# Kernel optimization log

Measured on AMD Instinct MI355X. Metric: run time of the kernel, lower is better.

The kernel has to match this reference:

```python
import jax, jax.numpy as jnp
import numpy as np

NL, H, PD, NH, NB = 4, 256, 64, 4, 65
B, L, AA = 2, 384, 48
DH = H // NH
MAX_REL = 32


def _ln(x, g, b):
    m = x.mean(-1, keepdims=True)
    v = ((x - m) ** 2).mean(-1, keepdims=True)
    return (x - m) * jax.lax.rsqrt(v + 1e-5) * g + b


def setup_inputs() -> dict:
    key = jax.random.key(0)
    ks = iter(jax.random.split(key, 64))
    w = lambda *s: jax.random.normal(next(ks), s, jnp.float32) * 0.02
    return dict(
        x=jax.random.normal(next(ks), (B, L, AA), jnp.float32),
        rp_w=w(AA, H), rp_b=jnp.zeros((H,), jnp.float32),
        pos_embed=w(L, H),
        pii_w=w(H, PD), pii_b=jnp.zeros((PD,), jnp.float32),
        pij_w=w(H, PD), pij_b=jnp.zeros((PD,), jnp.float32),
        rel_emb=w(2 * MAX_REL + 2, PD),
        ln_seq_g=jnp.ones((NL, H), jnp.float32), ln_seq_b=jnp.zeros((NL, H), jnp.float32),
        ln_pair_g=jnp.ones((NL, PD), jnp.float32), ln_pair_b=jnp.zeros((NL, PD), jnp.float32),
        pb_w=w(NL, PD, NH),
        in_w=w(NL, H, 3 * H), in_b=jnp.zeros((NL, 3 * H), jnp.float32),
        out_w=w(NL, H, H), out_b=jnp.zeros((NL, H), jnp.float32),
        ff_ln_g=jnp.ones((NL, H), jnp.float32), ff_ln_b=jnp.zeros((NL, H), jnp.float32),
        ff_w1=w(NL, H, 4 * H), ff_b1=jnp.zeros((NL, 4 * H), jnp.float32),
        ff_w2=w(NL, 4 * H, H), ff_b2=jnp.zeros((NL, H), jnp.float32),
        pu_ln_g=jnp.ones((NL, PD), jnp.float32), pu_ln_b=jnp.zeros((NL, PD), jnp.float32),
        pu_w1=w(NL, PD, PD), pu_b1=jnp.zeros((NL, PD), jnp.float32),
        pu_w2=w(NL, PD, PD), pu_b2=jnp.zeros((NL, PD), jnp.float32),
        outer_w=w(NL, 2 * H, PD), outer_b=jnp.zeros((NL, PD), jnp.float32),
        dh_ln_g=jnp.ones((PD,), jnp.float32), dh_ln_b=jnp.zeros((PD,), jnp.float32),
        dh_w1=w(PD, PD), dh_b1=jnp.zeros((PD,), jnp.float32),
        dh_w2=w(PD, NB), dh_b2=jnp.zeros((NB,), jnp.float32),
    )


def reference(x, rp_w, rp_b, pos_embed, pii_w, pii_b, pij_w, pij_b, rel_emb,
              ln_seq_g, ln_seq_b, ln_pair_g, ln_pair_b, pb_w, in_w, in_b,
              out_w, out_b, ff_ln_g, ff_ln_b, ff_w1, ff_b1, ff_w2, ff_b2,
              pu_ln_g, pu_ln_b, pu_w1, pu_b1, pu_w2, pu_b2, outer_w, outer_b,
              dh_ln_g, dh_ln_b, dh_w1, dh_b1, dh_w2, dh_b2):
    Bx, Lx, _ = x.shape
    gelu = lambda t: jax.nn.gelu(t, approximate=False)  # torch nn.GELU default (erf)
    h = x @ rp_w + rp_b + pos_embed[:Lx][None]
    # pair init: outer sum of two linear projections + clipped rel-pos embedding
    pair = (h @ pii_w + pii_b)[:, :, None, :] + (h @ pij_w + pij_b)[:, None, :, :]
    idx = jnp.arange(Lx)
    rel = jnp.clip(idx[None, :] - idx[:, None], -MAX_REL, MAX_REL) + MAX_REL  # (L,L)
    pair = pair + rel_emb[rel][None]
    for i in range(NL):
        seq_n = _ln(h, ln_seq_g[i], ln_seq_b[i])
        bias = _ln(pair, ln_pair_g[i], ln_pair_b[i]) @ pb_w[i]  # (B,L,L,NH)
        mask = bias.mean(axis=(0, 3))  # torch: permute->reshape(B*NH,L,L)->mean(0)
        qkv = seq_n @ in_w[i] + in_b[i]
        q, k, v = jnp.split(qkv, 3, axis=-1)
        q = q.reshape(Bx, Lx, NH, DH)
        k = k.reshape(Bx, Lx, NH, DH)
        v = v.reshape(Bx, Lx, NH, DH)
        scores = jnp.einsum('blhd,bmhd->bhlm', q, k) / float(np.sqrt(DH)) + mask
        attn = jax.nn.softmax(scores, axis=-1)
        o = jnp.einsum('bhlm,bmhd->blhd', attn, v).reshape(Bx, Lx, H)
        h = h + o @ out_w[i] + out_b[i]
        h = h + gelu(_ln(h, ff_ln_g[i], ff_ln_b[i]) @ ff_w1[i] + ff_b1[i]) @ ff_w2[i] + ff_b2[i]
        # outer_proj(cat([h_i, h_j])) == h@W[:H] outer-summed with h@W[H:]
        oi = h @ outer_w[i][:H]
        oj = h @ outer_w[i][H:]
        outer = oi[:, :, None, :] + oj[:, None, :, :] + outer_b[i]  # (B,L,L,PD)
        pair = pair + gelu(_ln(outer, pu_ln_g[i], pu_ln_b[i]) @ pu_w1[i] + pu_b1[i]) @ pu_w2[i] + pu_b2[i]
    logits = gelu(_ln(pair, dh_ln_g, dh_ln_b) @ dh_w1 + dh_b1) @ dh_w2 + dh_b2
    return (logits + jnp.swapaxes(logits, 1, 2)) / 2.0
```

## Files before the change

### kernel.cpp

```cpp
#include <hip/hip_runtime.h>
#include <math.h>

#define LSEQ 384
#define HD 256
#define PDIM 64
#define NHEAD 4
#define NBINS 65
#define BATCH 2
#define NTT (LSEQ / 16)
#define NTRI (NTT * (NTT + 1) / 2)

typedef __attribute__((ext_vector_type(8))) short bf16x8;
typedef __attribute__((ext_vector_type(16))) float f32x16;
#define MFMA32(a, b, c) __builtin_amdgcn_mfma_f32_32x32x16_bf16(a, b, c, 0, 0, 0)

template<int CTRL, int RMASK>
__device__ __forceinline__ float dpp_sum_step(float v) {
    int x = __builtin_amdgcn_update_dpp(0, __float_as_int(v), CTRL, RMASK, 0xf, true);
    return v + __int_as_float(x);
}
template<int CTRL, int RMASK>
__device__ __forceinline__ float dpp_max_step(float v) {
    int x = __builtin_amdgcn_update_dpp(__float_as_int(v), __float_as_int(v), CTRL, RMASK, 0xf, false);
    return fmaxf(v, __int_as_float(x));
// ... 42 lines not shown
    int t = threadIdx.x;
    if (t < 48) xs[t] = x[row * 48 + t];
    __syncthreads();
    float acc = rp_b[t] + pos[l * HD + t];
#pragma unroll 8
    for (int a = 0; a < 48; ++a) acc += xs[a] * rp_w[a * HD + t];
    h[row * HD + t] = acc;
}

__global__ void k_proj2(const float* __restrict__ h, const float* __restrict__ wA,
                        const float* __restrict__ wB, const float* __restrict__ bA,
                        const float* __restrict__ bB, int center,
                        float* __restrict__ pA, float* __restrict__ pB) {
    __shared__ float hs[HD];
    int row = blockIdx.x;
    int t = threadIdx.x;
    hs[t] = h[row * HD + t];
    hs[t + 128] = h[row * HD + t + 128];
    __syncthreads();
    int col = t & 63;
    const float* w = (t < 64) ? wA : wB;
    const float* bias = (t < 64) ? bA : bB;
    float acc = bias ? bias[col] : 0.0f;
#pragma unroll 8
    for (int a = 0; a < HD; ++a) acc += hs[a] * w[a * PDIM + col];
    if (center) {
        float mean = wsum(acc) * (1.0f / PDIM);
        acc -= mean;
    }
    float* p = (t < 64) ? pA : pB;
    p[row * PDIM + col] = acc;
}

__global__ void k_pair_init(const float* __restrict__ pi, const float* __restrict__ pj,
                            const float* __restrict__ rel_emb, float* __restrict__ pair) {
    __shared__ float pis[PDIM];
    int row = blockIdx.x;
    int b = row / LSEQ, i = row % LSEQ;
    int t = threadIdx.x;
    if (t < PDIM) pis[t] = pi[row * PDIM + t];
    __syncthreads();
    const float* pjb = pj + (size_t)b * LSEQ * PDIM;
    float* pr = pair + (size_t)row * LSEQ * PDIM;
    for (int n = t; n < LSEQ * PDIM; n += 256) {
        int j = n >> 6, d = n & 63;
        int r = j - i; r = r < -32 ? -32 : (r > 32 ? 32 : r); r += 32;
        pr[n] = pis[d] + pjb[j * PDIM + d] + rel_emb[r * PDIM + d];
    }
}

__global__ void k_prep(const float* __restrict__ pu_ln_g, const float* __restrict__ pu_ln_b,
                       const float* __restrict__ pu_w1, const float* __restrict__ pu_b1,
                       const float* __restrict__ pu_w2,
                       const float* __restrict__ dh_ln_g, const float* __restrict__ dh_ln_b,
                       const float* __restrict__ dh_w1, const float* __restrict__ dh_b1,
                       const float* __restrict__ dh_w2,
                       unsigned short* __restrict__ w1hT, unsigned short* __restrict__ w1lT,
                       unsigned short* __restrict__ w2hT, unsigned short* __restrict__ w2lT,
                       float* __restrict__ b1p, float* __restrict__ w2c) {
    int i = blockIdx.x;
    int c = threadIdx.x;
    const float *g, *bb, *w1, *b1, *w2;
    int w2s;
    if (i < 4) { g = pu_ln_g + i * 64; bb = pu_ln_b + i * 64; w1 = pu_w1 + i * 4096;
                 b1 = pu_b1 + i * 64; w2 = pu_w2 + i * 4096; w2s = 64; }
    else       { g = dh_ln_g; bb = dh_ln_b; w1 = dh_w1; b1 = dh_b1; w2 = dh_w2; w2s = 65; }
    float accb = b1[c];
    for (int k = 0; k < 64; ++k) {
        float wv = w1[k * 64 + c];
        accb += bb[k] * wv;
        unsigned short h, l;
        split_bf(g[k] * wv, h, l);
        w1hT[i * 4096 + c * 64 + k] = h;
        w1lT[i * 4096 + c * 64 + k] = l;
        split_bf(w2[k * w2s + c], h, l);
        w2hT[i * 4096 + c * 64 + k] = h;
        w2lT[i * 4096 + c * 64 + k] = l;
    }
    b1p[i * 64 + c] = accb;
    if (i == 4) w2c[c] = dh_w2[c * 65 + 64];
}

__global__ void k_maskprep(const float* __restrict__ g, const float* __restrict__ bb,
                           const float* __restrict__ pbw, float* __restrict__ gp,
                           float* __restrict__ cb) {
    int li = blockIdx.x + 1;
    int c = threadIdx.x;
    const float* pw = pbw + li * PDIM * NHEAD;
    float pbs = pw[c * 4] + pw[c * 4 + 1] + pw[c * 4 + 2] + pw[c * 4 + 3];
    gp[blockIdx.x * 64 + c] = g[li * 64 + c] * pbs;
    float s = wsum(bb[li * 64 + c] * pbs);
    if (c == 0) cb[blockIdx.x] = s;
}

__global__ void k_split_T(const float* __restrict__ src, unsigned short* __restrict__ dh,
                          unsigned short* __restrict__ dl, int K, int N,
                          int tiles_k, int tiles_n, size_t sstride, size_t dstride) {
    __shared__ float lds[64][65];
    int bid = blockIdx.x;
    int tpl = tiles_k * tiles_n;
    int layer = bid / tpl;
    int rest = bid % tpl;
    int kt = rest / tiles_n, nt = rest % tiles_n;
    const float* s = src + layer * sstride;
    int t = threadIdx.x, c = t & 63, r0 = t >> 6;
    for (int r = r0; r < 64; r += 4)
        lds[r][c] = s[(size_t)(kt * 64 + r) * N + nt * 64 + c];
    __syncthreads();
    unsigned short* oh = dh + layer * dstride;
    unsigned short* ol = dl + layer * dstride;
    for (int r = r0; r < 64; r += 4) {
        float v = lds[c][r];
        unsigned short h, l;
        split_bf(v, h, l);
        size_t o = (size_t)(nt * 64 + r) * K + kt * 64 + c;
        oh[o] = h;
        ol[o] = l;
    }
}

template<bool GELU>
__global__ void __launch_bounds__(256) k_gemm(
    const float* __restrict__ X, const unsigned short* __restrict__ wTh,
    const unsigned short* __restrict__ wTl, const float* __restrict__ bias,
    const float* __restrict__ R, float* __restrict__ OUT, int K, int N) {
// ... 6 lines not shown
    const unsigned short* bh = wTh + (size_t)(nt * 32 + pl) * K + 8 * hq;
    const unsigned short* bl = wTl + (size_t)(nt * 32 + pl) * K + 8 * hq;
    int n = nt * 32 + pl;
    float bv = bias[n];
    f32x16 acc;
#pragma unroll
    for (int r = 0; r < 16; ++r) {
        int mr = mt * 32 + (r & 3) + 8 * (r >> 2) + 4 * hq;
        acc[r] = bv + (R ? R[(size_t)mr * N + n] : 0.0f);
    }
#pragma unroll 4
    for (int s = 0; s < K; s += 16) {
        bf16x8 ah, al;
#pragma unroll
        for (int j = 0; j < 8; ++j) {
            unsigned short h, l;
            split_bf(xr[s + j], h, l);
            ah[j] = (short)h; al[j] = (short)l;
        }
        bf16x8 bhv = *(const bf16x8*)(bh + s);
        bf16x8 blv = *(const bf16x8*)(bl + s);
        acc = MFMA32(ah, bhv, acc);
        acc = MFMA32(al, bhv, acc);
        acc = MFMA32(ah, blv, acc);
    }
#pragma unroll
    for (int r = 0; r < 16; ++r) {
        int mr = mt * 32 + (r & 3) + 8 * (r >> 2) + 4 * hq;
        float v = acc[r];
        OUT[(size_t)mr * N + n] = GELU ? gelu_erf(v) : v;
    }
}

__global__ void k_mask(const float* __restrict__ pair, const float* __restrict__ g,
                       const float* __restrict__ bb, const float* __restrict__ pbw,
                       float* __restrict__ mask) {
    int wid = (blockIdx.x * 4 + (threadIdx.x >> 6)) * 2;
    int lane = threadIdx.x & 63;
    int l = wid / LSEQ, m0 = wid % LSEQ;
    float gd = g[lane], bd = bb[lane];
    float pbs = pbw[lane * 4] + pbw[lane * 4 + 1] + pbw[lane * 4 + 2] + pbw[lane * 4 + 3];
    float v[4];
#pragma unroll
    for (int s = 0; s < 4; ++s) {
        int b = s >> 1, m = m0 + (s & 1);
        v[s] = pair[(((size_t)(b * LSEQ + l)) * LSEQ + m) * PDIM + lane];
    }
    float mean[4], d[4], var[4], dot[4];
#pragma unroll
    for (int s = 0; s < 4; ++s) mean[s] = wsum(v[s]) * (1.0f / PDIM);
#pragma unroll
    for (int s = 0; s < 4; ++s) d[s] = v[s] - mean[s];
#pragma unroll
    for (int s = 0; s < 4; ++s) var[s] = wsum(d[s] * d[s]) * (1.0f / PDIM);
#pragma unroll
    for (int s = 0; s < 4; ++s) {
        float ln = d[s] * rsqrtf(var[s] + 1e-5f) * gd + bd;
        dot[s] = wsum(ln * pbs);
    }
    if (lane == 0) {
        mask[l * LSEQ + m0]     = (dot[0] + dot[2]) * (1.0f / (BATCH * NHEAD));
        mask[l * LSEQ + m0 + 1] = (dot[1] + dot[3]) * (1.0f / (BATCH * NHEAD));
    }
}

__global__ void k_ln_seq(const float* __restrict__ h, const float* __restrict__ g,
                         const float* __restrict__ b, float* __restrict__ out) {
    __shared__ float red[8];
    int row = blockIdx.x;
    int t = threadIdx.x;
    int w = t >> 6, lane = t & 63;
    float v = h[row * HD + t];
    float s = wsum(v);
    if (lane == 0) red[w] = s;
    __syncthreads();
    float mean = (red[0] + red[1] + red[2] + red[3]) * (1.0f / HD);
    float d = v - mean;
    float q = wsum(d * d);
    if (lane == 0) red[4 + w] = q;
    __syncthreads();
    float var = (red[4] + red[5] + red[6] + red[7]) * (1.0f / HD);
    out[row * HD + t] = d * rsqrtf(var + 1e-5f) * g[t] + b[t];
}

__global__ void k_attn(const float* __restrict__ qkv, const float* __restrict__ mask,
                       float* __restrict__ o) {
    __shared__ __align__(16) float qs[64];
    __shared__ float sc[LSEQ];
    __shared__ float red[8];
    __shared__ float op[4][64];
    int bid = blockIdx.x;
    int l = bid % LSEQ;
    int nh = (bid / LSEQ) & 3;
    int b = bid / (LSEQ * NHEAD);
    int t = threadIdx.x;
    int w = t >> 6, lane = t & 63;
    const float* qbase = qkv + ((size_t)(b * LSEQ + l)) * 768 + nh * 64;
    if (t < 64) qs[t] = qbase[t];
// ... 18 lines not shown
            lmax = fmaxf(lmax, s);
        } else myv[it] = -1e30f;
    }
    float wm = wmax(lmax);
    if (lane == 0) red[w] = wm;
    __syncthreads();
    float gmax = fmaxf(fmaxf(red[0], red[1]), fmaxf(red[2], red[3]));
    float lsum = 0.0f;
#pragma unroll
    for (int it = 0; it < 2; ++it) {
        int m = t + it * 256;
        if (m < LSEQ) {
            float e = expf(myv[it] - gmax);
            sc[m] = e;
            lsum += e;
        }
    }
    float ws = wsum(lsum);
    if (lane == 0) red[4 + w] = ws;
    __syncthreads();
    float inv = 1.0f / (red[4] + red[5] + red[6] + red[7]);
    int d = t & 63, gq = t >> 6;
    float part = 0.0f;
    for (int m = gq * 96; m < (gq + 1) * 96; ++m)
        part += sc[m] * qkv[((size_t)(b * LSEQ + m)) * 768 + 512 + nh * 64 + d];
    op[gq][d] = part;
    __syncthreads();
    if (t < 64) {
        float ov = (op[0][t] + op[1][t] + op[2][t] + op[3][t]) * inv;
        o[((size_t)(b * LSEQ + l)) * HD + nh * 64 + t] = ov;
    }
}

__global__ void __launch_bounds__(256) k_pair_upd(
    const float* __restrict__ ojc,
    const float* __restrict__ oic,
    const unsigned short* __restrict__ w1hT, const unsigned short* __restrict__ w1lT,
    const float* __restrict__ b1p,
    const unsigned short* __restrict__ w2hT, const unsigned short* __restrict__ w2lT,
    const float* __restrict__ b2, float* __restrict__ pair,
    const float* __restrict__ gpb, const float* __restrict__ cbv,
    float* __restrict__ mask_out) {
    __shared__ float pt[128][65];
    __shared__ float gpl[64];
    int blk = blockIdx.x;
    int row = blk / 3, seg = blk % 3;
    int b = row / LSEQ;
    int t = threadIdx.x;
    int wave = t >> 6, lane = t & 63;
    int pl = lane & 31, hq = lane >> 5;
    int pv = wave * 32 + pl;
    int p = seg * 128 + pv;
    const float* ojr = ojc + ((size_t)b * LSEQ + p) * 64;
    const float* oir = oic + (size_t)row * 64;
    float* prblk = pair + ((size_t)row * LSEQ + seg * 128) * 64;

    const float4* src4 = (const float4*)prblk;
    for (int n = t; n < 2048; n += 256) {
        float4 g4 = src4[n];
        int pv2 = n >> 4, ch = (n & 15) << 2;
        pt[pv2][ch] = g4.x; pt[pv2][ch + 1] = g4.y;
        pt[pv2][ch + 2] = g4.z; pt[pv2][ch + 3] = g4.w;
    }
    if (mask_out && t < 64) gpl[t] = gpb[t];

    float v[32];
#pragma unroll
    for (int s = 0; s < 4; ++s) {
        int k0 = 16 * s + 8 * hq;
#pragma unroll
        for (int j = 0; j < 8; ++j) v[8 * s + j] = ojr[k0 + j] + oir[k0 + j];
    }
    float ss = 0.0f;
#pragma unroll
    for (int i = 0; i < 32; ++i) ss = fmaf(v[i], v[i], ss);
    ss += __shfl_xor(ss, 32);
    float rs = rsqrtf(ss * (1.0f / PDIM) + 1e-5f);
    bf16x8 zh[4], zl[4];
#pragma unroll
    for (int s = 0; s < 4; ++s)
#pragma unroll
        for (int j = 0; j < 8; ++j) {
            unsigned short h, l;
            split_bf(v[8 * s + j] * rs, h, l);
            zh[s][j] = (short)h; zl[s][j] = (short)l;
        }

    f32x16 acc0, acc1;
#pragma unroll
    for (int r = 0; r < 16; ++r) {
        int rr = (r & 3) + 8 * (r >> 2) + 4 * hq;
        acc0[r] = b1p[rr];
        acc1[r] = b1p[32 + rr];
    }
#pragma unroll
    for (int s = 0; s < 4; ++s) {
        int ko = 16 * s + 8 * hq;
// ... 12 lines not shown
#pragma unroll
    for (int r = 0; r < 16; ++r) { u0[r] = gelu_erf(acc0[r]); u1[r] = gelu_erf(acc1[r]); }

    float rA0[4], rB0[4], rA1[4], rB1[4];
#pragma unroll
    for (int i = 0; i < 4; ++i) {
        rA0[i] = __shfl_xor(hq ? u0[i] : u0[4 + i], 32);
        rB0[i] = __shfl_xor(hq ? u0[8 + i] : u0[12 + i], 32);
        rA1[i] = __shfl_xor(hq ? u1[i] : u1[4 + i], 32);
        rB1[i] = __shfl_xor(hq ? u1[8 + i] : u1[12 + i], 32);
    }
    bf16x8 uh[4], ul[4];
#pragma unroll
    for (int s = 0; s < 4; ++s) {
        int tt = s >> 1, q = s & 1;
#pragma unroll
        for (int i = 0; i < 4; ++i) {
            float own_f = q ? (tt ? u1[8 + i] : u0[8 + i]) : (tt ? u1[i] : u0[i]);
            float own_s = q ? (tt ? u1[12 + i] : u0[12 + i]) : (tt ? u1[4 + i] : u0[4 + i]);
            float rcv   = q ? (tt ? rB1[i] : rB0[i]) : (tt ? rA1[i] : rA0[i]);
            float f  = hq ? rcv : own_f;
            float g2 = hq ? own_s : rcv;
            unsigned short h, l;
            split_bf(f, h, l);  uh[s][i] = (short)h;     ul[s][i] = (short)l;
            split_bf(g2, h, l); uh[s][4 + i] = (short)h; ul[s][4 + i] = (short)l;
        }
    }

    __syncthreads();
    f32x16 c0, c1;
#pragma unroll
    for (int r = 0; r < 16; ++r) {
        int rr = (r & 3) + 8 * (r >> 2) + 4 * hq;
        c0[r] = b2[rr] + pt[pv][rr];
        c1[r] = b2[32 + rr] + pt[pv][32 + rr];
    }
#pragma unroll
    for (int s = 0; s < 4; ++s) {
        int ko = 16 * s + 8 * hq;
        bf16x8 a0h = *(const bf16x8*)(w2hT + (pl << 6) + ko);
        bf16x8 a0l = *(const bf16x8*)(w2lT + (pl << 6) + ko);
        bf16x8 a1h = *(const bf16x8*)(w2hT + ((32 + pl) << 6) + ko);
        bf16x8 a1l = *(const bf16x8*)(w2lT + ((32 + pl) << 6) + ko);
        c0 = MFMA32(a0h, uh[s], c0);
        c0 = MFMA32(a0h, ul[s], c0);
        c0 = MFMA32(a0l, uh[s], c0);
        c1 = MFMA32(a1h, uh[s], c1);
        c1 = MFMA32(a1h, ul[s], c1);
        c1 = MFMA32(a1l, uh[s], c1);
    }
#pragma unroll
    for (int r = 0; r < 16; ++r) {
        int rr = (r & 3) + 8 * (r >> 2) + 4 * hq;
        pt[pv][rr] = c0[r];
        pt[pv][32 + rr] = c1[r];
    }
    if (mask_out) {
        float sv = 0.0f;
#pragma unroll
        for (int r = 0; r < 16; ++r) sv += c0[r] + c1[r];
        sv += __shfl_xor(sv, 32);
        float mean = sv * (1.0f / PDIM);
        float sd2 = 0.0f, sdg = 0.0f;
#pragma unroll 4
        for (int r = 0; r < 16; ++r) {
            int rr = (r & 3) + 8 * (r >> 2) + 4 * hq;
            float d0 = c0[r] - mean, d1 = c1[r] - mean;
            sd2 = fmaf(d0, d0, sd2);
            sd2 = fmaf(d1, d1, sd2);
            sdg = fmaf(d0, gpl[rr], sdg);
            sdg = fmaf(d1, gpl[32 + rr], sdg);
        }
        sd2 += __shfl_xor(sd2, 32);
        sdg += __shfl_xor(sdg, 32);
        float rsv = rsqrtf(sd2 * (1.0f / PDIM) + 1e-5f);
        float dot = rsv * sdg + cbv[0];
        if (hq == 0)
            atomicAdd(mask_out + (row % LSEQ) * LSEQ + p, dot * (1.0f / (BATCH * NHEAD)));
    }
    __syncthreads();
    float4* dst4 = (float4*)prblk;
    for (int n = t; n < 2048; n += 256) {
        int pv2 = n >> 4, ch = (n & 15) << 2;
        float4 g4 = { pt[pv2][ch], pt[pv2][ch + 1], pt[pv2][ch + 2], pt[pv2][ch + 3] };
        dst4[n] = g4;
    }
}

__global__ void __launch_bounds__(256) k_dist(
    const float* __restrict__ pair,
    const unsigned short* __restrict__ w1hT, const unsigned short* __restrict__ w1lT,
    const float* __restrict__ b1p,
    const unsigned short* __restrict__ w2hT, const unsigned short* __restrict__ w2lT,
    const float* __restrict__ w2c, const float* __restrict__ b2,
    float* __restrict__ out) {
    __shared__ __align__(16) float ot[128][NBINS];
    int blk = blockIdx.x;
    int row = blk / 3, seg = blk % 3;
    int t = threadIdx.x;
    int wave = t >> 6, lane = t & 63;
    int pl = lane & 31, hq = lane >> 5;
    int pv = wave * 32 + pl;
    int p = seg * 128 + pv;
    const float* prp = pair + ((size_t)row * LSEQ + p) * 64;
    float v[32];
#pragma unroll
    for (int s = 0; s < 4; ++s) {
        int k0 = 16 * s + 8 * hq;
#pragma unroll
        for (int j = 0; j < 8; ++j) v[8 * s + j] = prp[k0 + j];
    }
    float sm = 0.0f;
#pragma unroll
    for (int i = 0; i < 32; ++i) sm += v[i];
    sm += __shfl_xor(sm, 32);
    float mean = sm * (1.0f / PDIM);
    float ss = 0.0f;
#pragma unroll
    for (int i = 0; i < 32; ++i) { v[i] -= mean; ss = fmaf(v[i], v[i], ss); }
    ss += __shfl_xor(ss, 32);
    float rs = rsqrtf(ss * (1.0f / PDIM) + 1e-5f);
    bf16x8 zh[4], zl[4];
#pragma unroll
    for (int s = 0; s < 4; ++s)
#pragma unroll
        for (int j = 0; j < 8; ++j) {
            unsigned short h, l;
            split_bf(v[8 * s + j] * rs, h, l);
            zh[s][j] = (short)h; zl[s][j] = (short)l;
        }
    f32x16 acc0, acc1;
#pragma unroll
    for (int r = 0; r < 16; ++r) {
        int rr = (r & 3) + 8 * (r >> 2) + 4 * hq;
        acc0[r] = b1p[rr];
        acc1[r] = b1p[32 + rr];
    }
#pragma unroll
    for (int s = 0; s < 4; ++s) {
        int ko = 16 * s + 8 * hq;
        bf16x8 a0h = *(const bf16x8*)(w1hT + (pl << 6) + ko);
        bf16x8 a0l = *(const bf16x8*)(w1lT + (pl << 6) + ko);
        bf16x8 a1h = *(const bf16x8*)(w1hT + ((32 + pl) << 6) + ko);
        bf16x8 a1l = *(const bf16x8*)(w1lT + ((32 + pl) << 6) + ko);
        acc0 = MFMA32(a0h, zh[s], acc0);
        acc0 = MFMA32(a0h, zl[s], acc0);
        acc0 = MFMA32(a0l, zh[s], acc0);
        acc1 = MFMA32(a1h, zh[s], acc1);
        acc1 = MFMA32(a1h, zl[s], acc1);
        acc1 = MFMA32(a1l, zh[s], acc1);
    }
    float u0[16], u1[16];
    float p64 = 0.0f;
#pragma unroll
    for (int r = 0; r < 16; ++r) {
        int rr = (r & 3) + 8 * (r >> 2) + 4 * hq;
        u0[r] = gelu_erf(acc0[r]);
        u1[r] = gelu_erf(acc1[r]);
        p64 = fmaf(u0[r], w2c[rr], p64);
        p64 = fmaf(u1[r], w2c[32 + rr], p64);
    }
    p64 += __shfl_xor(p64, 32);
    float rA0[4], rB0[4], rA1[4], rB1[4];
#pragma unroll
    for (int i = 0; i < 4; ++i) {
        rA0[i] = __shfl_xor(hq ? u0[i] : u0[4 + i], 32);
        rB0[i] = __shfl_xor(hq ? u0[8 + i] : u0[12 + i], 32);
        rA1[i] = __shfl_xor(hq ? u1[i] : u1[4 + i], 32);
        rB1[i] = __shfl_xor(hq ? u1[8 + i] : u1[12 + i], 32);
    }
    bf16x8 uh[4], ul[4];
#pragma unroll
    for (int s = 0; s < 4; ++s) {
        int tt = s >> 1, q = s & 1;
#pragma unroll
        for (int i = 0; i < 4; ++i) {
            float own_f = q ? (tt ? u1[8 + i] : u0[8 + i]) : (tt ? u1[i] : u0[i]);
            float own_s = q ? (tt ? u1[12 + i] : u0[12 + i]) : (tt ? u1[4 + i] : u0[4 + i]);
            float rcv   = q ? (tt ? rB1[i] : rB0[i]) : (tt ? rA1[i] : rA0[i]);
            float f  = hq ? rcv : own_f;
            float g2 = hq ? own_s : rcv;
            unsigned short h, l;
            split_bf(f, h, l);  uh[s][i] = (short)h;     ul[s][i] = (short)l;
            split_bf(g2, h, l); uh[s][4 + i] = (short)h; ul[s][4 + i] = (short)l;
        }
    }
    f32x16 c0, c1;
#pragma unroll
    for (int r = 0; r < 16; ++r) {
        int rr = (r & 3) + 8 * (r >> 2) + 4 * hq;
        c0[r] = b2[rr];
        c1[r] = b2[32 + rr];
    }
#pragma unroll
    for (int s = 0; s < 4; ++s) {
        int ko = 16 * s + 8 * hq;
        bf16x8 a0h = *(const bf16x8*)(w2hT + (pl << 6) + ko);
        bf16x8 a0l = *(const bf16x8*)(w2lT + (pl << 6) + ko);
        bf16x8 a1h = *(const bf16x8*)(w2hT + ((32 + pl) << 6) + ko);
        bf16x8 a1l = *(const bf16x8*)(w2lT + ((32 + pl) << 6) + ko);
        c0 = MFMA32(a0h, uh[s], c0);
        c0 = MFMA32(a0h, ul[s], c0);
        c0 = MFMA32(a0l, uh[s], c0);
        c1 = MFMA32(a1h, uh[s], c1);
        c1 = MFMA32(a1h, ul[s], c1);
        c1 = MFMA32(a1l, uh[s], c1);
    }
#pragma unroll
    for (int r = 0; r < 16; ++r) {
        int rr = (r & 3) + 8 * (r >> 2) + 4 * hq;
        ot[pv][rr] = c0[r];
        ot[pv][32 + rr] = c1[r];
    }
    if (hq == 0) ot[pv][64] = p64 + b2[64];
    __syncthreads();
    float4* dst = (float4*)(out + ((size_t)row * LSEQ + seg * 128) * NBINS);
    const float4* src = (const float4*)&ot[0][0];
    for (int n = t; n < 128 * NBINS / 4; n += 256) dst[n] = src[n];
}

__global__ void k_sym(float* __restrict__ out) {
    int u = blockIdx.x;
    int b = 0;
    if (u >= NTRI) { b = 1; u -= NTRI; }
    int lt = 0, rem = NTT;
    while (u >= rem) { u -= rem; ++lt; --rem; }
    int mt = lt + u;
    int t = threadIdx.x;
    int g = t >> 6, lane = t & 63;
    float* ob = out + (size_t)b * LSEQ * LSEQ * NBINS;
    for (int e = g; e < 256; e += 4) {
        int i = e >> 4, j = e & 15;
        if (lt == mt && j < i) continue;
        size_t ia = ((size_t)(lt * 16 + i) * LSEQ + (mt * 16 + j)) * NBINS;
        size_t ib = ((size_t)(mt * 16 + j) * LSEQ + (lt * 16 + i)) * NBINS;
        for (int k = lane; k < NBINS; k += 64) {
            float a = ob[ia + k], c = ob[ib + k];
            float vv = 0.5f * (a + c);
            ob[ia + k] = vv;
            if (ia != ib) ob[ib + k] = vv;
        }
    }
}

extern "C" void kernel_launch(void* const* d_in, const int* in_sizes, int n_in,
                              void* d_out, int out_size, void* d_ws, size_t ws_size,
                              hipStream_t stream) {
    const float* x        = (const float*)d_in[0];
    const float* rp_w     = (const float*)d_in[1];
    const float* rp_b     = (const float*)d_in[2];
    const float* pos      = (const float*)d_in[3];
// ... 15 lines not shown
    const float* ff_ln_b  = (const float*)d_in[19];
    const float* ff_w1    = (const float*)d_in[20];
    const float* ff_b1    = (const float*)d_in[21];
    const float* ff_w2    = (const float*)d_in[22];
    const float* ff_b2    = (const float*)d_in[23];
    const float* pu_ln_g  = (const float*)d_in[24];
    const float* pu_ln_b  = (const float*)d_in[25];
    const float* pu_w1    = (const float*)d_in[26];
    const float* pu_b1    = (const float*)d_in[27];
    const float* pu_w2    = (const float*)d_in[28];
    const float* pu_b2    = (const float*)d_in[29];
    const float* outer_w  = (const float*)d_in[30];
    const float* outer_b  = (const float*)d_in[31];
    const float* dh_ln_g  = (const float*)d_in[32];
    const float* dh_ln_b  = (const float*)d_in[33];
    const float* dh_w1    = (const float*)d_in[34];
    const float* dh_b1    = (const float*)d_in[35];
    const float* dh_w2    = (const float*)d_in[36];
    const float* dh_b2    = (const float*)d_in[37];
    float* outp = (float*)d_out;

    float* W = (float*)d_ws;
    float* h    = W;  W += BATCH * LSEQ * HD;
    float* sn   = W;  W += BATCH * LSEQ * HD;
    float* qkv  = W;  W += BATCH * LSEQ * 3 * HD;
    float* ob   = W;  W += BATCH * LSEQ * HD;
    float* mid  = W;  W += BATCH * LSEQ * 4 * HD;
    float* maskA= W;  W += LSEQ * LSEQ;
    float* maskB= W;  W += LSEQ * LSEQ;
    float* poi  = W;  W += BATCH * LSEQ * PDIM;
    float* poj  = W;  W += BATCH * LSEQ * PDIM;
    float* b1p  = W;  W += 5 * 64;
    float* w2c  = W;  W += 64;
    float* gpb  = W;  W += 3 * 64;
    float* cbv  = W;  W += 64;
    unsigned short* w1hT = (unsigned short*)W;  W += 5 * 2048;
    unsigned short* w1lT = (unsigned short*)W;  W += 5 * 2048;
    unsigned short* w2hT = (unsigned short*)W;  W += 5 * 2048;
    unsigned short* w2lT = (unsigned short*)W;  W += 5 * 2048;
    unsigned short* qwT_h = (unsigned short*)W;  W += 4 * 196608 / 2;
    unsigned short* qwT_l = (unsigned short*)W;  W += 4 * 196608 / 2;
    unsigned short* owT_h = (unsigned short*)W;  W += 4 * 65536 / 2;
    unsigned short* owT_l = (unsigned short*)W;  W += 4 * 65536 / 2;
    unsigned short* f1T_h = (unsigned short*)W;  W += 4 * 262144 / 2;
    unsigned short* f1T_l = (unsigned short*)W;  W += 4 * 262144 / 2;
    unsigned short* f2T_h = (unsigned short*)W;  W += 4 * 262144 / 2;
    unsigned short* f2T_l = (unsigned short*)W;  W += 4 * 262144 / 2;
    float* pair = W;  W += (size_t)BATCH * LSEQ * LSEQ * PDIM;

    const int rows = BATCH * LSEQ;

    k_prep<<<5, 64, 0, stream>>>(pu_ln_g, pu_ln_b, pu_w1, pu_b1, pu_w2,
                                 dh_ln_g, dh_ln_b, dh_w1, dh_b1, dh_w2,
                                 w1hT, w1lT, w2hT, w2lT, b1p, w2c);
    k_maskprep<<<3, 64, 0, stream>>>(ln_pair_g, ln_pair_b, pb_w, gpb, cbv);
    k_split_T<<<4 * 4 * 12, 256, 0, stream>>>(in_w,  qwT_h, qwT_l, 256, 768,  4, 12, 196608, 196608);
    k_split_T<<<4 * 4 * 4,  256, 0, stream>>>(out_w, owT_h, owT_l, 256, 256,  4, 4,  65536,  65536);
    k_split_T<<<4 * 4 * 16, 256, 0, stream>>>(ff_w1, f1T_h, f1T_l, 256, 1024, 4, 16, 262144, 262144);
    k_split_T<<<4 * 16 * 4, 256, 0, stream>>>(ff_w2, f2T_h, f2T_l, 1024, 256, 16, 4, 262144, 262144);
    k_h_init<<<rows, 256, 0, stream>>>(x, rp_w, rp_b, pos, h);
    k_proj2<<<rows, 128, 0, stream>>>(h, pii_w, pij_w, pii_b, pij_b, 0, poi, poj);
    k_pair_init<<<rows, 256, 0, stream>>>(poi, poj, rel_emb, pair);
    k_mask<<<LSEQ * LSEQ / 8, 256, 0, stream>>>(pair, ln_pair_g, ln_pair_b, pb_w, maskA);

    float* mcur = maskA;
    float* mnext = maskB;
    for (int i = 0; i < 4; ++i) {
        k_ln_seq<<<rows, 256, 0, stream>>>(h, ln_seq_g + i * HD, ln_seq_b + i * HD, sn);
        k_gemm<false><<<144, 256, 0, stream>>>(sn, qwT_h + i * 196608, qwT_l + i * 196608,
                                               in_b + i * 768, nullptr, qkv, 256, 768);
        k_attn<<<BATCH * NHEAD * LSEQ, 256, 0, stream>>>(qkv, mcur, ob);
        k_gemm<false><<<48, 256, 0, stream>>>(ob, owT_h + i * 65536, owT_l + i * 65536,
                                              out_b + i * 256, h, h, 256, 256);
        k_ln_seq<<<rows, 256, 0, stream>>>(h, ff_ln_g + i * HD, ff_ln_b + i * HD, sn);
        k_gemm<true><<<192, 256, 0, stream>>>(sn, f1T_h + i * 262144, f1T_l + i * 262144,
                                              ff_b1 + i * 1024, nullptr, mid, 256, 1024);
        k_gemm<false><<<48, 256, 0, stream>>>(mid, f2T_h + i * 262144, f2T_l + i * 262144,
                                              ff_b2 + i * 256, h, h, 1024, 256);
        k_proj2<<<rows, 128, 0, stream>>>(h, outer_w + i * 2 * HD * PDIM,
                                          outer_w + i * 2 * HD * PDIM + HD * PDIM,
                                          outer_b + i * PDIM, nullptr, 1, poi, poj);
        if (i < 3)
            hipMemsetAsync(mnext, 0, LSEQ * LSEQ * sizeof(float), stream);
        k_pair_upd<<<rows * 3, 256, 0, stream>>>(poj, poi,
                                                 w1hT + i * 4096, w1lT + i * 4096,
                                                 b1p + i * 64,
                                                 w2hT + i * 4096, w2lT + i * 4096,
                                                 pu_b2 + i * PDIM, pair,
                                                 (i < 3) ? gpb + i * 64 : nullptr,
                                                 (i < 3) ? cbv + i : nullptr,
                                                 (i < 3) ? mnext : nullptr);
        float* tmp = mcur; mcur = mnext; mnext = tmp;
    }

    k_dist<<<rows * 3, 256, 0, stream>>>(pair, w1hT + 4 * 4096, w1lT + 4 * 4096,
                                         b1p + 4 * 64, w2hT + 4 * 4096, w2lT + 4 * 4096,
                                         w2c, dh_b2, outp);
    k_sym<<<2 * NTRI, 256, 0, stream>>>(outp);
}
```

Baseline: 1.221 ms.

## Fuse initial mask into pair init and distance head into last pair update

Pair init now also computes the layer-0 attention mask from values still in LDS, so the separate mask kernel that reread the full pair tensor is gone. The last layer's pair update is templated to run the distance head directly on its result, which drops the final pair write-back and the separate k_dist pass over the pair tensor. Blocks shrink from 256 to 64 threads with 32 positions each, giving four times as many blocks. This trades some per-block overhead and weight-fragment reloads for less global memory traffic and fewer launches.

```diff
diff --git a/kernel.cpp b/kernel.cpp
--- a/kernel.cpp
+++ b/kernel.cpp
@@ -98,21 +98,51 @@
     p[row * PDIM + col] = acc;
 }
 
-__global__ void k_pair_init(const float* __restrict__ pi, const float* __restrict__ pj,
-                            const float* __restrict__ rel_emb, float* __restrict__ pair) {
-    __shared__ float pis[PDIM];
-    int row = blockIdx.x;
+__global__ void __launch_bounds__(64) k_pair_init2(
+    const float* __restrict__ pi, const float* __restrict__ pj,
+    const float* __restrict__ rel_emb, const float* __restrict__ gpb,
+    const float* __restrict__ cbv, float* __restrict__ pair,
+    float* __restrict__ mask_out) {
+    __shared__ __align__(16) float pt[32][65];
+    int blk = blockIdx.x;
+    int row = blk / 12, seg = blk % 12;
     int b = row / LSEQ, i = row % LSEQ;
     int t = threadIdx.x;
-    if (t < PDIM) pis[t] = pi[row * PDIM + t];
-    __syncthreads();
-    const float* pjb = pj + (size_t)b * LSEQ * PDIM;
-    float* pr = pair + (size_t)row * LSEQ * PDIM;
-    for (int n = t; n < LSEQ * PDIM; n += 256) {
-        int j = n >> 6, d = n & 63;
-        int r = j - i; r = r < -32 ? -32 : (r > 32 ? 32 : r); r += 32;
-        pr[n] = pis[d] + pjb[j * PDIM + d] + rel_emb[r * PDIM + d];
-    }
+    int pl = t & 31, hq = t >> 5;
+    int j0 = seg * 32;
+    float piv = pi[row * 64 + t];
+    const float* pjb = pj + ((size_t)b * LSEQ + j0) * 64;
+#pragma unroll 8
+    for (int j = 0; j < 32; ++j) {
+        int r = j0 + j - i; r = r < -32 ? -32 : (r > 32 ? 32 : r); r += 32;
+        pt[j][t] = piv + pjb[j * 64 + t] + rel_emb[r * 64 + t];
+    }
+    __syncthreads();
+    float4* dst4 = (float4*)(pair + ((size_t)row * LSEQ + j0) * 64);
+    for (int n = t; n < 512; n += 64) {
+        int r2 = n >> 4, c4 = (n & 15) << 2;
+        float4 g4 = { pt[r2][c4], pt[r2][c4 + 1], pt[r2][c4 + 2], pt[r2][c4 + 3] };
+        dst4[n] = g4;
+    }
+    float vv[32];
+    float sv = 0.0f;
+#pragma unroll
+    for (int c = 0; c < 32; ++c) { vv[c] = pt[pl][hq * 32 + c]; sv += vv[c]; }
+    sv += __shfl_xor(sv, 32);
+    float mean = sv * (1.0f / PDIM);
+    float sd2 = 0.0f, sdg = 0.0f;
+#pragma unroll
+    for (int c = 0; c < 32; ++c) {
+        float d = vv[c] - mean;
+        sd2 = fmaf(d, d, sd2);
+        sdg = fmaf(d, gpb[hq * 32 + c], sdg);
+    }
+    sd2 += __shfl_xor(sd2, 32);
+    sdg += __shfl_xor(sdg, 32);
+    float rsv = rsqrtf(sd2 * (1.0f / PDIM) + 1e-5f);
+    float dot = rsv * sdg + cbv[0];
+    if (hq == 0)
+        atomicAdd(mask_out + i * LSEQ + j0 + pl, dot * (1.0f / (BATCH * NHEAD)));
 }
 
 __global__ void k_prep(const float* __restrict__ pu_ln_g, const float* __restrict__ pu_ln_b,
@@ -150,13 +180,13 @@
 __global__ void k_maskprep(const float* __restrict__ g, const float* __restrict__ bb,
                            const float* __restrict__ pbw, float* __restrict__ gp,
                            float* __restrict__ cb) {
-    int li = blockIdx.x + 1;
+    int li = blockIdx.x;
     int c = threadIdx.x;
     const float* pw = pbw + li * PDIM * NHEAD;
     float pbs = pw[c * 4] + pw[c * 4 + 1] + pw[c * 4 + 2] + pw[c * 4 + 3];
-    gp[blockIdx.x * 64 + c] = g[li * 64 + c] * pbs;
+    gp[li * 64 + c] = g[li * 64 + c] * pbs;
     float s = wsum(bb[li * 64 + c] * pbs);
-    if (c == 0) cb[blockIdx.x] = s;
+    if (c == 0) cb[li] = s;
 }
 
 __global__ void k_split_T(const float* __restrict__ src, unsigned short* __restrict__ dh,
@@ -229,38 +259,6 @@
     }
 }
 
-__global__ void k_mask(const float* __restrict__ pair, const float* __restrict__ g,
-                       const float* __restrict__ bb, const float* __restrict__ pbw,
-                       float* __restrict__ mask) {
-    int wid = (blockIdx.x * 4 + (threadIdx.x >> 6)) * 2;
-    int lane = threadIdx.x & 63;
-    int l = wid / LSEQ, m0 = wid % LSEQ;
-    float gd = g[lane], bd = bb[lane];
-    float pbs = pbw[lane * 4] + pbw[lane * 4 + 1] + pbw[lane * 4 + 2] + pbw[lane * 4 + 3];
-    float v[4];
-#pragma unroll
-    for (int s = 0; s < 4; ++s) {
-        int b = s >> 1, m = m0 + (s & 1);
-        v[s] = pair[(((size_t)(b * LSEQ + l)) * LSEQ + m) * PDIM + lane];
-    }
-    float mean[4], d[4], var[4], dot[4];
-#pragma unroll
-    for (int s = 0; s < 4; ++s) mean[s] = wsum(v[s]) * (1.0f / PDIM);
-#pragma unroll
-    for (int s = 0; s < 4; ++s) d[s] = v[s] - mean[s];
-#pragma unroll
-    for (int s = 0; s < 4; ++s) var[s] = wsum(d[s] * d[s]) * (1.0f / PDIM);
-#pragma unroll
-    for (int s = 0; s < 4; ++s) {
-        float ln = d[s] * rsqrtf(var[s] + 1e-5f) * gd + bd;
-        dot[s] = wsum(ln * pbs);
-    }
-    if (lane == 0) {
-        mask[l * LSEQ + m0]     = (dot[0] + dot[2]) * (1.0f / (BATCH * NHEAD));
-        mask[l * LSEQ + m0 + 1] = (dot[1] + dot[3]) * (1.0f / (BATCH * NHEAD));
-    }
-}
-
 __global__ void k_ln_seq(const float* __restrict__ h, const float* __restrict__ g,
                          const float* __restrict__ b, float* __restrict__ out) {
     __shared__ float red[8];
@@ -345,7 +343,8 @@
     }
 }
 
-__global__ void __launch_bounds__(256) k_pair_upd(
+template<bool DIST>
+__global__ void __launch_bounds__(64) k_pair_upd(
     const float* __restrict__ ojc,
     const float* __restrict__ oic,
     const unsigned short* __restrict__ w1hT, const unsigned short* __restrict__ w1lT,
@@ -353,29 +352,30 @@
     const unsigned short* __restrict__ w2hT, const unsigned short* __restrict__ w2lT,
     const float* __restrict__ b2, float* __restrict__ pair,
     const float* __restrict__ gpb, const float* __restrict__ cbv,
-    float* __restrict__ mask_out) {
-    __shared__ float pt[128][65];
-    __shared__ float gpl[64];
+    float* __restrict__ mask_out,
+    const unsigned short* __restrict__ dw1h, const unsigned short* __restrict__ dw1l,
+    const float* __restrict__ db1p,
+    const unsigned short* __restrict__ dw2h, const unsigned short* __restrict__ dw2l,
+    const float* __restrict__ w2c, const float* __restrict__ db2,
+    float* __restrict__ outg) {
+    __shared__ __align__(16) float pt[32][65];
     int blk = blockIdx.x;
-    int row = blk / 3, seg = blk % 3;
+    int row = blk / 12, seg = blk % 12;
     int b = row / LSEQ;
     int t = threadIdx.x;
-    int wave = t >> 6, lane = t & 63;
-    int pl = lane & 31, hq = lane >> 5;
-    int pv = wave * 32 + pl;
-    int p = seg * 128 + pv;
+    int pl = t & 31, hq = t >> 5;
+    int p = seg * 32 + pl;
     const float* ojr = ojc + ((size_t)b * LSEQ + p) * 64;
     const float* oir = oic + (size_t)row * 64;
-    float* prblk = pair + ((size_t)row * LSEQ + seg * 128) * 64;
+    float* prblk = pair + ((size_t)row * LSEQ + seg * 32) * 64;
 
     const float4* src4 = (const float4*)prblk;
-    for (int n = t; n < 2048; n += 256) {
+    for (int n = t; n < 512; n += 64) {
         float4 g4 = src4[n];
-        int pv2 = n >> 4, ch = (n & 15) << 2;
-        pt[pv2][ch] = g4.x; pt[pv2][ch + 1] = g4.y;
-        pt[pv2][ch + 2] = g4.z; pt[pv2][ch + 3] = g4.w;
-    }
-    if (mask_out && t < 64) gpl[t] = gpb[t];
+        int r2 = n >> 4, ch = (n & 15) << 2;
+        pt[r2][ch] = g4.x; pt[r2][ch + 1] = g4.y;
+        pt[r2][ch + 2] = g4.z; pt[r2][ch + 3] = g4.w;
+    }
 
     float v[32];
 #pragma unroll
@@ -454,8 +454,8 @@
 #pragma unroll
     for (int r = 0; r < 16; ++r) {
         int rr = (r & 3) + 8 * (r >> 2) + 4 * hq;
-        c0[r] = b2[rr] + pt[pv][rr];
-        c1[r] = b2[32 + rr] + pt[pv][32 + rr];
+        c0[r] = b2[rr] + pt[pl][rr];
+        c1[r] = b2[32 + rr] + pt[pl][32 + rr];
     }
 #pragma unroll
     for (int s = 0; s < 4; ++s) {
@@ -471,174 +471,162 @@
         c1 = MFMA32(a1h, ul[s], c1);
         c1 = MFMA32(a1l, uh[s], c1);
     }
-#pragma unroll
-    for (int r = 0; r < 16; ++r) {
-        int rr = (r & 3) + 8 * (r >> 2) + 4 * hq;
-        pt[pv][rr] = c0[r];
-        pt[pv][32 + rr] = c1[r];
-    }
-    if (mask_out) {
-        float sv = 0.0f;
-#pragma unroll
-        for (int r = 0; r < 16; ++r) sv += c0[r] + c1[r];
-        sv += __shfl_xor(sv, 32);
-        float mean = sv * (1.0f / PDIM);
-        float sd2 = 0.0f, sdg = 0.0f;
-#pragma unroll 4
+
+    if constexpr (!DIST) {
+#pragma unroll
         for (int r = 0; r < 16; ++r) {
             int rr = (r & 3) + 8 * (r >> 2) + 4 * hq;
-            float d0 = c0[r] - mean, d1 = c1[r] - mean;
-            sd2 = fmaf(d0, d0, sd2);
-            sd2 = fmaf(d1, d1, sd2);
-            sdg = fmaf(d0, gpl[rr], sdg);
-            sdg = fmaf(d1, gpl[32 + rr], sdg);
-        }
-        sd2 += __shfl_xor(sd2, 32);
-        sdg += __shfl_xor(sdg, 32);
-        float rsv = rsqrtf(sd2 * (1.0f / PDIM) + 1e-5f);
-        float dot = rsv * sdg + cbv[0];
-        if (hq == 0)
-            atomicAdd(mask_out + (row % LSEQ) * LSEQ + p, dot * (1.0f / (BATCH * NHEAD)));
-    }
-    __syncthreads();
-    float4* dst4 = (float4*)prblk;
-    for (int n = t; n < 2048; n += 256) {
-        int pv2 = n >> 4, ch = (n & 15) << 2;
-        float4 g4 = { pt[pv2][ch], pt[pv2][ch + 1], pt[pv2][ch + 2], pt[pv2][ch + 3] };
-        dst4[n] = g4;
-    }
-}
-
-__global__ void __launch_bounds__(256) k_dist(
-    const float* __restrict__ pair,
-    const unsigned short* __restrict__ w1hT, const unsigned short* __restrict__ w1lT,
-    const float* __restrict__ b1p,
-    const unsigned short* __restrict__ w2hT, const unsigned short* __restrict__ w2lT,
-    const float* __restrict__ w2c, const float* __restrict__ b2,
-    float* __restrict__ out) {
-    __shared__ __align__(16) float ot[128][NBINS];
-    int blk = blockIdx.x;
-    int row = blk / 3, seg = blk % 3;
-    int t = threadIdx.x;
-    int wave = t >> 6, lane = t & 63;
-    int pl = lane & 31, hq = lane >> 5;
-    int pv = wave * 32 + pl;
-    int p = seg * 128 + pv;
-    const float* prp = pair + ((size_t)row * LSEQ + p) * 64;
-    float v[32];
-#pragma unroll
-    for (int s = 0; s < 4; ++s) {
-        int k0 = 16 * s + 8 * hq;
-#pragma unroll
-        for (int j = 0; j < 8; ++j) v[8 * s + j] = prp[k0 + j];
-    }
-    float sm = 0.0f;
-#pragma unroll
-    for (int i = 0; i < 32; ++i) sm += v[i];
-    sm += __shfl_xor(sm, 32);
-    float mean = sm * (1.0f / PDIM);
-    float ss = 0.0f;
-#pragma unroll
-    for (int i = 0; i < 32; ++i) { v[i] -= mean; ss = fmaf(v[i], v[i], ss); }
-    ss += __shfl_xor(ss, 32);
-    float rs = rsqrtf(ss * (1.0f / PDIM) + 1e-5f);
-    bf16x8 zh[4], zl[4];
-#pragma unroll
-    for (int s = 0; s < 4; ++s)
-#pragma unroll
-        for (int j = 0; j < 8; ++j) {
-            unsigned short h, l;
-            split_bf(v[8 * s + j] * rs, h, l);
-            zh[s][j] = (short)h; zl[s][j] = (short)l;
-        }
-    f32x16 acc0, acc1;
-#pragma unroll
-    for (int r = 0; r < 16; ++r) {
-        int rr = (r & 3) + 8 * (r >> 2) + 4 * hq;
-        acc0[r] = b1p[rr];
-        acc1[r] = b1p[32 + rr];
-    }
-#pragma unroll
-    for (int s = 0; s < 4; ++s) {
-        int ko = 16 * s + 8 * hq;
-        bf16x8 a0h = *(const bf16x8*)(w1hT + (pl << 6) + ko);
-        bf16x8 a0l = *(const bf16x8*)(w1lT + (pl << 6) + ko);
-        bf16x8 a1h = *(const bf16x8*)(w1hT + ((32 + pl) << 6) + ko);
-        bf16x8 a1l = *(const bf16x8*)(w1lT + ((32 + pl) << 6) + ko);
-        acc0 = MFMA32(a0h, zh[s], acc0);
-        acc0 = MFMA32(a0h, zl[s], acc0);
-        acc0 = MFMA32(a0l, zh[s], acc0);
-        acc1 = MFMA32(a1h, zh[s], acc1);
-        acc1 = MFMA32(a1h, zl[s], acc1);
-        acc1 = MFMA32(a1l, zh[s], acc1);
-    }
-    float u0[16], u1[16];
-    float p64 = 0.0f;
-#pragma unroll
-    for (int r = 0; r < 16; ++r) {
-        int rr = (r & 3) + 8 * (r >> 2) + 4 * hq;
-        u0[r] = gelu_erf(acc0[r]);
-        u1[r] = gelu_erf(acc1[r]);
-        p64 = fmaf(u0[r], w2c[rr], p64);
-        p64 = fmaf(u1[r], w2c[32 + rr], p64);
-    }
-    p64 += __shfl_xor(p64, 32);
-    float rA0[4], rB0[4], rA1[4], rB1[4];
-#pragma unroll
-    for (int i = 0; i < 4; ++i) {
-        rA0[i] = __shfl_xor(hq ? u0[i] : u0[4 + i], 32);
-        rB0[i] = __shfl_xor(hq ? u0[8 + i] : u0[12 + i], 32);
-        rA1[i] = __shfl_xor(hq ? u1[i] : u1[4 + i], 32);
-        rB1[i] = __shfl_xor(hq ? u1[8 + i] : u1[12 + i], 32);
-    }
-    bf16x8 uh[4], ul[4];
-#pragma unroll
-    for (int s = 0; s < 4; ++s) {
-        int tt = s >> 1, q = s & 1;
+            pt[pl][rr] = c0[r];
+            pt[pl][32 + rr] = c1[r];
+        }
+        if (mask_out) {
+            float sv = 0.0f;
+#pragma unroll
+            for (int r = 0; r < 16; ++r) sv += c0[r] + c1[r];
+            sv += __shfl_xor(sv, 32);
+            float mean = sv * (1.0f / PDIM);
+            float sd2 = 0.0f, sdg = 0.0f;
+#pragma unroll 4
+            for (int r = 0; r < 16; ++r) {
+                int rr = (r & 3) + 8 * (r >> 2) + 4 * hq;
+                float d0 = c0[r] - mean, d1 = c1[r] - mean;
+                sd2 = fmaf(d0, d0, sd2);
+                sd2 = fmaf(d1, d1, sd2);
+                sdg = fmaf(d0, gpb[rr], sdg);
+                sdg = fmaf(d1, gpb[32 + rr], sdg);
+            }
+            sd2 += __shfl_xor(sd2, 32);
+            sdg += __shfl_xor(sdg, 32);
+            float rsv = rsqrtf(sd2 * (1.0f / PDIM) + 1e-5f);
+            float dot = rsv * sdg + cbv[0];
+            if (hq == 0)
+                atomicAdd(mask_out + (row % LSEQ) * LSEQ + p, dot * (1.0f / (BATCH * NHEAD)));
+        }
+        __syncthreads();
+        float4* dst4 = (float4*)prblk;
+        for (int n = t; n < 512; n += 64) {
+            int r2 = n >> 4, ch = (n & 15) << 2;
+            float4 g4 = { pt[r2][ch], pt[r2][ch + 1], pt[r2][ch + 2], pt[r2][ch + 3] };
+            dst4[n] = g4;
+        }
+    } else {
+#pragma unroll
+        for (int r = 0; r < 16; ++r) {
+            int rr = (r & 3) + 8 * (r >> 2) + 4 * hq;
+            pt[pl][rr] = c0[r];
+            pt[pl][32 + rr] = c1[r];
+        }
+        __syncthreads();
+        float v2[32];
+#pragma unroll
+        for (int s = 0; s < 4; ++s) {
+            int k0 = 16 * s + 8 * hq;
+#pragma unroll
+            for (int j = 0; j < 8; ++j) v2[8 * s + j] = pt[pl][k0 + j];
+        }
+        float sm = 0.0f;
+#pragma unroll
+        for (int i = 0; i < 32; ++i) sm += v2[i];
+        sm += __shfl_xor(sm, 32);
+        float mean = sm * (1.0f / PDIM);
+        float ss2 = 0.0f;
+#pragma unroll
+        for (int i = 0; i < 32; ++i) { v2[i] -= mean; ss2 = fmaf(v2[i], v2[i], ss2); }
+        ss2 += __shfl_xor(ss2, 32);
+        float rs2 = rsqrtf(ss2 * (1.0f / PDIM) + 1e-5f);
+#pragma unroll
+        for (int s = 0; s < 4; ++s)
+#pragma unroll
+            for (int j = 0; j < 8; ++j) {
+                unsigned short h, l;
+                split_bf(v2[8 * s + j] * rs2, h, l);
+                zh[s][j] = (short)h; zl[s][j] = (short)l;
+            }
+#pragma unroll
+        for (int r = 0; r < 16; ++r) {
+            int rr = (r & 3) + 8 * (r >> 2) + 4 * hq;
+            acc0[r] = db1p[rr];
+            acc1[r] = db1p[32 + rr];
+        }
+#pragma unroll
+        for (int s = 0; s < 4; ++s) {
+            int ko = 16 * s + 8 * hq;
+            bf16x8 a0h = *(const bf16x8*)(dw1h + (pl << 6) + ko);
+            bf16x8 a0l = *(const bf16x8*)(dw1l + (pl << 6) + ko);
+            bf16x8 a1h = *(const bf16x8*)(dw1h + ((32 + pl) << 6) + ko);
+            bf16x8 a1l = *(const bf16x8*)(dw1l + ((32 + pl) << 6) + ko);
+            acc0 = MFMA32(a0h, zh[s], acc0);
+            acc0 = MFMA32(a0h, zl[s], acc0);
+            acc0 = MFMA32(a0l, zh[s], acc0);
+            acc1 = MFMA32(a1h, zh[s], acc1);
+            acc1 = MFMA32(a1h, zl[s], acc1);
+            acc1 = MFMA32(a1l, zh[s], acc1);
+        }
+        float p64 = 0.0f;
+#pragma unroll
+        for (int r = 0; r < 16; ++r) {
+            int rr = (r & 3) + 8 * (r >> 2) + 4 * hq;
+            u0[r] = gelu_erf(acc0[r]);
+            u1[r] = gelu_erf(acc1[r]);
+            p64 = fmaf(u0[r], w2c[rr], p64);
+            p64 = fmaf(u1[r], w2c[32 + rr], p64);
+        }
+        p64 += __shfl_xor(p64, 32);
 #pragma unroll
         for (int i = 0; i < 4; ++i) {
-            float own_f = q ? (tt ? u1[8 + i] : u0[8 + i]) : (tt ? u1[i] : u0[i]);
-            float own_s = q ? (tt ? u1[12 + i] : u0[12 + i]) : (tt ? u1[4 + i] : u0[4 + i]);
-            float rcv   = q ? (tt ? rB1[i] : rB0[i]) : (tt ? rA1[i] : rA0[i]);
-            float f  = hq ? rcv : own_f;
-            float g2 = hq ? own_s : rcv;
-            unsigned short h, l;
-            split_bf(f, h, l);  uh[s][i] = (short)h;     ul[s][i] = (short)l;
-            split_bf(g2, h, l); uh[s][4 + i] = (short)h; ul[s][4 + i] = (short)l;
-        }
-    }
-    f32x16 c0, c1;
-#pragma unroll
-    for (int r = 0; r < 16; ++r) {
-        int rr = (r & 3) + 8 * (r >> 2) + 4 * hq;
-        c0[r] = b2[rr];
-        c1[r] = b2[32 + rr];
-    }
-#pragma unroll
-    for (int s = 0; s < 4; ++s) {
-        int ko = 16 * s + 8 * hq;
-        bf16x8 a0h = *(const bf16x8*)(w2hT + (pl << 6) + ko);
-        bf16x8 a0l = *(const bf16x8*)(w2lT + (pl << 6) + ko);
-        bf16x8 a1h = *(const bf16x8*)(w2hT + ((32 + pl) << 6) + ko);
-        bf16x8 a1l = *(const bf16x8*)(w2lT + ((32 + pl) << 6) + ko);
-        c0 = MFMA32(a0h, uh[s], c0);
-        c0 = MFMA32(a0h, ul[s], c0);
-        c0 = MFMA32(a0l, uh[s], c0);
-        c1 = MFMA32(a1h, uh[s], c1);
-        c1 = MFMA32(a1h, ul[s], c1);
-        c1 = MFMA32(a1l, uh[s], c1);
-    }
-#pragma unroll
-    for (int r = 0; r < 16; ++r) {
-        int rr = (r & 3) + 8 * (r >> 2) + 4 * hq;
-        ot[pv][rr] = c0[r];
-        ot[pv][32 + rr] = c1[r];
-    }
-    if (hq == 0) ot[pv][64] = p64 + b2[64];
-    __syncthreads();
-    float4* dst = (float4*)(out + ((size_t)row * LSEQ + seg * 128) * NBINS);
-    const float4* src = (const float4*)&ot[0][0];
-    for (int n = t; n < 128 * NBINS / 4; n += 256) dst[n] = src[n];
+            rA0[i] = __shfl_xor(hq ? u0[i] : u0[4 + i], 32);
+            rB0[i] = __shfl_xor(hq ? u0[8 + i] : u0[12 + i], 32);
+            rA1[i] = __shfl_xor(hq ? u1[i] : u1[4 + i], 32);
+            rB1[i] = __shfl_xor(hq ? u1[8 + i] : u1[12 + i], 32);
+        }
+#pragma unroll
+        for (int s = 0; s < 4; ++s) {
+            int tt = s >> 1, q = s & 1;
+#pragma unroll
+            for (int i = 0; i < 4; ++i) {
+                float own_f = q ? (tt ? u1[8 + i] : u0[8 + i]) : (tt ? u1[i] : u0[i]);
+                float own_s = q ? (tt ? u1[12 + i] : u0[12 + i]) : (tt ? u1[4 + i] : u0[4 + i]);
+                float rcv   = q ? (tt ? rB1[i] : rB0[i]) : (tt ? rA1[i] : rA0[i]);
+                float f  = hq ? rcv : own_f;
+                float g2 = hq ? own_s : rcv;
+                unsigned short h, l;
+                split_bf(f, h, l);  uh[s][i] = (short)h;     ul[s][i] = (short)l;
+                split_bf(g2, h, l); uh[s][4 + i] = (short)h; ul[s][4 + i] = (short)l;
+            }
+        }
+#pragma unroll
+        for (int r = 0; r < 16; ++r) {
+            int rr = (r & 3) + 8 * (r >> 2) + 4 * hq;
+            c0[r] = db2[rr];
+            c1[r] = db2[32 + rr];
+        }
+#pragma unroll
+        for (int s = 0; s < 4; ++s) {
+            int ko = 16 * s + 8 * hq;
+            bf16x8 a0h = *(const bf16x8*)(dw2h + (pl << 6) + ko);
+            bf16x8 a0l = *(const bf16x8*)(dw2l + (pl << 6) + ko);
+            bf16x8 a1h = *(const bf16x8*)(dw2h + ((32 + pl) << 6) + ko);
+            bf16x8 a1l = *(const bf16x8*)(dw2l + ((32 + pl) << 6) + ko);
+            c0 = MFMA32(a0h, uh[s], c0);
+            c0 = MFMA32(a0h, ul[s], c0);
+            c0 = MFMA32(a0l, uh[s], c0);
+            c1 = MFMA32(a1h, uh[s], c1);
+            c1 = MFMA32(a1h, ul[s], c1);
+            c1 = MFMA32(a1l, uh[s], c1);
+        }
+        __syncthreads();
+#pragma unroll
+        for (int r = 0; r < 16; ++r) {
+            int rr = (r & 3) + 8 * (r >> 2) + 4 * hq;
+            pt[pl][rr] = c0[r];
+            pt[pl][32 + rr] = c1[r];
+        }
+        if (hq == 0) pt[pl][64] = p64 + db2[64];
+        __syncthreads();
+        float4* dst = (float4*)(outg + ((size_t)row * LSEQ + seg * 32) * NBINS);
+        const float4* srcl = (const float4*)&pt[0][0];
+        for (int n = t; n < 520; n += 64) dst[n] = srcl[n];
+    }
 }
 
 __global__ void k_sym(float* __restrict__ out) {
@@ -720,7 +708,7 @@
     float* poj  = W;  W += BATCH * LSEQ * PDIM;
     float* b1p  = W;  W += 5 * 64;
     float* w2c  = W;  W += 64;
-    float* gpb  = W;  W += 3 * 64;
+    float* gpb  = W;  W += 4 * 64;
     float* cbv  = W;  W += 64;
     unsigned short* w1hT = (unsigned short*)W;  W += 5 * 2048;
     unsigned short* w1lT = (unsigned short*)W;  W += 5 * 2048;
@@ -741,15 +729,15 @@
     k_prep<<<5, 64, 0, stream>>>(pu_ln_g, pu_ln_b, pu_w1, pu_b1, pu_w2,
                                  dh_ln_g, dh_ln_b, dh_w1, dh_b1, dh_w2,
                                  w1hT, w1lT, w2hT, w2lT, b1p, w2c);
-    k_maskprep<<<3, 64, 0, stream>>>(ln_pair_g, ln_pair_b, pb_w, gpb, cbv);
+    k_maskprep<<<4, 64, 0, stream>>>(ln_pair_g, ln_pair_b, pb_w, gpb, cbv);
     k_split_T<<<4 * 4 * 12, 256, 0, stream>>>(in_w,  qwT_h, qwT_l, 256, 768,  4, 12, 196608, 196608);
     k_split_T<<<4 * 4 * 4,  256, 0, stream>>>(out_w, owT_h, owT_l, 256, 256,  4, 4,  65536,  65536);
     k_split_T<<<4 * 4 * 16, 256, 0, stream>>>(ff_w1, f1T_h, f1T_l, 256, 1024, 4, 16, 262144, 262144);
     k_split_T<<<4 * 16 * 4, 256, 0, stream>>>(ff_w2, f2T_h, f2T_l, 1024, 256, 16, 4, 262144, 262144);
     k_h_init<<<rows, 256, 0, stream>>>(x, rp_w, rp_b, pos, h);
     k_proj2<<<rows, 128, 0, stream>>>(h, pii_w, pij_w, pii_b, pij_b, 0, poi, poj);
-    k_pair_init<<<rows, 256, 0, stream>>>(poi, poj, rel_emb, pair);
-    k_mask<<<LSEQ * LSEQ / 8, 256, 0, stream>>>(pair, ln_pair_g, ln_pair_b, pb_w, maskA);
+    hipMemsetAsync(maskA, 0, LSEQ * LSEQ * sizeof(float), stream);
+    k_pair_init2<<<rows * 12, 64, 0, stream>>>(poi, poj, rel_emb, gpb, cbv, pair, maskA);
 
     float* mcur = maskA;
     float* mnext = maskB;
@@ -768,21 +756,25 @@
         k_proj2<<<rows, 128, 0, stream>>>(h, outer_w + i * 2 * HD * PDIM,
                                           outer_w + i * 2 * HD * PDIM + HD * PDIM,
                                           outer_b + i * PDIM, nullptr, 1, poi, poj);
-        if (i < 3)
+        if (i < 3) {
             hipMemsetAsync(mnext, 0, LSEQ * LSEQ * sizeof(float), stream);
-        k_pair_upd<<<rows * 3, 256, 0, stream>>>(poj, poi,
-                                                 w1hT + i * 4096, w1lT + i * 4096,
-                                                 b1p + i * 64,
-                                                 w2hT + i * 4096, w2lT + i * 4096,
-                                                 pu_b2 + i * PDIM, pair,
-                                                 (i < 3) ? gpb + i * 64 : nullptr,
-                                                 (i < 3) ? cbv + i : nullptr,
-                                                 (i < 3) ? mnext : nullptr);
-        float* tmp = mcur; mcur = mnext; mnext = tmp;
-    }
-
-    k_dist<<<rows * 3, 256, 0, stream>>>(pair, w1hT + 4 * 4096, w1lT + 4 * 4096,
-                                         b1p + 4 * 64, w2hT + 4 * 4096, w2lT + 4 * 4096,
-                                         w2c, dh_b2, outp);
+            k_pair_upd<false><<<rows * 12, 64, 0, stream>>>(
+                poj, poi,
+                w1hT + i * 4096, w1lT + i * 4096, b1p + i * 64,
+                w2hT + i * 4096, w2lT + i * 4096, pu_b2 + i * PDIM, pair,
+                gpb + (i + 1) * 64, cbv + (i + 1), mnext,
+                nullptr, nullptr, nullptr, nullptr, nullptr, nullptr, nullptr, nullptr);
+            float* tmp = mcur; mcur = mnext; mnext = tmp;
+        } else {
+            k_pair_upd<true><<<rows * 12, 64, 0, stream>>>(
+                poj, poi,
+                w1hT + 3 * 4096, w1lT + 3 * 4096, b1p + 3 * 64,
+                w2hT + 3 * 4096, w2lT + 3 * 4096, pu_b2 + 3 * PDIM, pair,
+                nullptr, nullptr, nullptr,
+                w1hT + 4 * 4096, w1lT + 4 * 4096, b1p + 4 * 64,
+                w2hT + 4 * 4096, w2lT + 4 * 4096, w2c, dh_b2, outp);
+        }
+    }
+
     k_sym<<<2 * NTRI, 256, 0, stream>>>(outp);
 }
```

Result: faster. 1.168 ms (-4.3%).
